# Kernel optimization log

Measured on AMD Instinct MI355X. Metric: run time of the kernel, lower is better.

## Reference

```python
import jax, jax.numpy as jnp
import numpy as np

B, T, DIN, DOUT, RANK, UDIM = 4, 2048, 4096, 4096, 2, 16

def setup_inputs() -> dict:
    key = jax.random.key(0)
    ks = jax.random.split(key, 8)
    return {
        "x": jax.random.normal(ks[0], (B, T, DIN), jnp.float32),
        "W": jax.random.normal(ks[1], (DOUT, DIN), jnp.float32) * 0.02,
        "b": jax.random.normal(ks[2], (DOUT,), jnp.float32) * 0.02,
        "U": jax.random.normal(ks[3], (DOUT, RANK), jnp.float32) * 0.02,
        "S": jax.random.normal(ks[4], (RANK, RANK), jnp.float32),
        "Vh": jax.random.normal(ks[5], (RANK, DIN), jnp.float32) * 0.02,
        "P": jax.random.normal(ks[6], (UDIM, RANK, RANK), jnp.float32),
        "v": jax.random.normal(ks[7], (UDIM,), jnp.float32),
    }

def reference(x, W, b, U, S, Vh, P, v):
    # R = sum_u v[u] * P[u]  (intended meaning of einsum('u,urr->rr'))
    R = jnp.einsum('u,uab->ab', v, P)                 # [rank, rank]
    base = jnp.einsum('btd,od->bto', x, W) + b        # frozen linear
    # x @ delta_W.T with delta_W = U @ S @ R @ Vh, chained low-rank:
    M = U @ S @ R                                     # [out, rank]
    t = jnp.einsum('btd,rd->btr', x, Vh)              # [B, T, rank]
    delta = jnp.einsum('btr,or->bto', t, M)           # [B, T, out]
    return base + delta
```

## Files before the change

### kernel.cpp

```cpp
#include <hip/hip_runtime.h>
#include <hip/hip_bf16.h>
#include <stdint.h>

typedef __hip_bfloat16 bf16;
typedef __attribute__((ext_vector_type(8))) short bf16x8;
typedef __attribute__((ext_vector_type(4))) float f32x4;

static constexpr int Mtot = 8192;
static constexpr int Ktot = 4096;
static constexpr int Ntot = 4096;
static constexpr int BM = 128, BN = 128, BK = 32;

__device__ __forceinline__ void gl_lds16(const void* g, void* l) {
  __builtin_amdgcn_global_load_lds(
      (const __attribute__((address_space(1))) void*)g,
      (__attribute__((address_space(3))) void*)l,
      16, 0, 0);
}

__device__ __forceinline__ uint32_t bf16pair(float a, float b) {
  __hip_bfloat16 ha = __float2bfloat16(a), hb = __float2bfloat16(b);
  uint16_t ia, ib;
  __builtin_memcpy(&ia, &ha, 2);
  __builtin_memcpy(&ib, &hb, 2);
  return (uint32_t)ia | ((uint32_t)ib << 16);
}

__global__ __launch_bounds__(256) void cast_x_kernel(const float* __restrict__ x,
                                                     bf16* __restrict__ xb) {
  size_t gid = (size_t)blockIdx.x * blockDim.x + threadIdx.x;
  size_t d0 = gid * 8;
  const float4 a = ((const float4*)(x + d0))[0];
  const float4 b = ((const float4*)(x + d0))[1];
  uint4 pk;
  pk.x = bf16pair(a.x, a.y);
  pk.y = bf16pair(a.z, a.w);
  pk.z = bf16pair(b.x, b.y);
  pk.w = bf16pair(b.z, b.w);
  ((uint4*)(xb + d0))[0] = pk;
}

__global__ __launch_bounds__(256) void prep_w_kernel(const float* __restrict__ W,
                                                     const float* __restrict__ U,
                                                     const float* __restrict__ S,
                                                     const float* __restrict__ Vh,
                                                     const float* __restrict__ P,
                                                     const float* __restrict__ v,
                                                     bf16* __restrict__ Wp) {
  float R0 = 0.f, R1 = 0.f, R2 = 0.f, R3 = 0.f;
#pragma unroll
  for (int u = 0; u < 16; ++u) {
    float vu = v[u];
    R0 += vu * P[u * 4 + 0];
    R1 += vu * P[u * 4 + 1];
    R2 += vu * P[u * 4 + 2];
    R3 += vu * P[u * 4 + 3];
  }
  float SR00 = S[0] * R0 + S[1] * R2, SR01 = S[0] * R1 + S[1] * R3;
  float SR10 = S[2] * R0 + S[3] * R2, SR11 = S[2] * R1 + S[3] * R3;

  int gid = blockIdx.x * blockDim.x + threadIdx.x;
  int o = gid >> 9;
  int d0 = (gid & 511) << 3;
  float u0 = U[o * 2 + 0], u1 = U[o * 2 + 1];
  float M0 = u0 * SR00 + u1 * SR10;
  float M1 = u0 * SR01 + u1 * SR11;

  const float* wrow = W + (size_t)o * Ktot + d0;
  const float* vh0 = Vh + d0;
  const float* vh1 = Vh + Ktot + d0;
  float val[8];
  const float4 w0 = ((const float4*)wrow)[0];
  const float4 w1 = ((const float4*)wrow)[1];
  const float4 a0 = ((const float4*)vh0)[0];
  const float4 a1 = ((const float4*)vh0)[1];
  const float4 b0 = ((const float4*)vh1)[0];
  const float4 b1 = ((const float4*)vh1)[1];
  val[0] = w0.x + M0 * a0.x + M1 * b0.x;
  val[1] = w0.y + M0 * a0.y + M1 * b0.y;
  val[2] = w0.z + M0 * a0.z + M1 * b0.z;
  val[3] = w0.w + M0 * a0.w + M1 * b0.w;
  val[4] = w1.x + M0 * a1.x + M1 * b1.x;
  val[5] = w1.y + M0 * a1.y + M1 * b1.y;
  val[6] = w1.z + M0 * a1.z + M1 * b1.z;
  val[7] = w1.w + M0 * a1.w + M1 * b1.w;
  uint4 pk;
  pk.x = bf16pair(val[0], val[1]);
  pk.y = bf16pair(val[2], val[3]);
  pk.z = bf16pair(val[4], val[5]);
  pk.w = bf16pair(val[6], val[7]);
  ((uint4*)(Wp + (size_t)o * Ktot + d0))[0] = pk;
}

__global__ __launch_bounds__(256) void gemm_kernel(const bf16* __restrict__ A,
                                                   const bf16* __restrict__ Bt,
                                                   const float* __restrict__ bias,
                                                   float* __restrict__ out) {
  __shared__ __align__(16) bf16 As[BM * BK];
  __shared__ __align__(16) bf16 Bs[BN * BK];

  const int tid = threadIdx.x;
  const int lane = tid & 63;
  const int wv = tid >> 6;
  const int m0 = blockIdx.y * BM;
  const int n0 = blockIdx.x * BN;

  const int lrow = lane >> 2;
  const int lk = (lane & 3) << 3;

  const bf16* ga0 = A + (size_t)(m0 + wv * 32 + lrow) * Ktot + lk;
  const bf16* ga1 = ga0 + (size_t)16 * Ktot;
  const bf16* gb0 = Bt + (size_t)(n0 + wv * 32 + lrow) * Ktot + lk;
  const bf16* gb1 = gb0 + (size_t)16 * Ktot;
  bf16* la0 = &As[(wv * 32) * BK];
  bf16* la1 = &As[(wv * 32 + 16) * BK];
  bf16* lb0 = &Bs[(wv * 32) * BK];
  bf16* lb1 = &Bs[(wv * 32 + 16) * BK];

  const int moff = (wv >> 1) * 64;
  const int noff = (wv & 1) * 64;
  const int fm = lane & 15;
  const int q = lane >> 4;
  const bf16* ra = &As[(moff + fm) * BK + q * 8];
  const bf16* rb = &Bs[(noff + fm) * BK + q * 8];

  f32x4 acc[4][4];
#pragma unroll
  for (int i = 0; i < 4; ++i)
#pragma unroll
    for (int j = 0; j < 4; ++j) acc[i][j] = {0.f, 0.f, 0.f, 0.f};

  for (int kt = 0; kt < Ktot / BK; ++kt) {
    gl_lds16(ga0, la0);
    gl_lds16(ga1, la1);
    gl_lds16(gb0, lb0);
    gl_lds16(gb1, lb1);
    ga0 += BK; ga1 += BK; gb0 += BK; gb1 += BK;
    __syncthreads();

    bf16x8 av[4], bv[4];
#pragma unroll
    for (int i = 0; i < 4; ++i) av[i] = *(const bf16x8*)(ra + i * 16 * BK);
#pragma unroll
    for (int j = 0; j < 4; ++j) bv[j] = *(const bf16x8*)(rb + j * 16 * BK);
#pragma unroll
    for (int i = 0; i < 4; ++i)
#pragma unroll
      for (int j = 0; j < 4; ++j)
        acc[i][j] = __builtin_amdgcn_mfma_f32_16x16x32_bf16(av[i], bv[j], acc[i][j], 0, 0, 0);
    __syncthreads();
  }

#pragma unroll
  for (int j = 0; j < 4; ++j) {
    const int gn = n0 + noff + j * 16 + fm;
    const float bj = bias[gn];
#pragma unroll
    for (int i = 0; i < 4; ++i) {
      const int gm = m0 + moff + i * 16 + q * 4;
#pragma unroll
      for (int r = 0; r < 4; ++r) {
        out[(size_t)(gm + r) * Ntot + gn] = acc[i][j][r] + bj;
      }
    }
  }
}

extern "C" void kernel_launch(void* const* d_in, const int* in_sizes, int n_in,
                              void* d_out, int out_size, void* d_ws, size_t ws_size,
                              hipStream_t stream) {
  const float* x  = (const float*)d_in[0];
  const float* W  = (const float*)d_in[1];
  const float* b  = (const float*)d_in[2];
  const float* U  = (const float*)d_in[3];
  const float* S  = (const float*)d_in[4];
  const float* Vh = (const float*)d_in[5];
  const float* P  = (const float*)d_in[6];
  const float* v  = (const float*)d_in[7];
  float* out = (float*)d_out;

  bf16* xb = (bf16*)d_ws;
  bf16* Wp = (bf16*)((char*)d_ws + (size_t)Mtot * Ktot * 2);

  cast_x_kernel<<<(Mtot * Ktot / 8) / 256, 256, 0, stream>>>(x, xb);
  prep_w_kernel<<<(Ntot * Ktot / 8) / 256, 256, 0, stream>>>(W, U, S, Vh, P, v, Wp);

  dim3 grid(Ntot / BN, Mtot / BM);
  gemm_kernel<<<grid, 256, 0, stream>>>(xb, Wp, b, out);
}
```

Before: 625.7 us.

## Double-buffer GEMM LDS tiles, XOR-swizzle LDS layout, merge prep kernels

```diff
diff --git a/kernel.cpp b/kernel.cpp
--- a/kernel.cpp
+++ b/kernel.cpp
@@ -10,6 +10,9 @@
 static constexpr int Ktot = 4096;
 static constexpr int Ntot = 4096;
 static constexpr int BM = 128, BN = 128, BK = 32;
+static constexpr int NK = Ktot / BK;
+static constexpr int CAST_BLOCKS = (Mtot * Ktot / 8) / 256;
+static constexpr int PREP_BLOCKS = (Ntot * Ktot / 8) / 256;
 
 __device__ __forceinline__ void gl_lds16(const void* g, void* l) {
   __builtin_amdgcn_global_load_lds(
@@ -26,78 +29,78 @@
   return (uint32_t)ia | ((uint32_t)ib << 16);
 }
 
-__global__ __launch_bounds__(256) void cast_x_kernel(const float* __restrict__ x,
-                                                     bf16* __restrict__ xb) {
-  size_t gid = (size_t)blockIdx.x * blockDim.x + threadIdx.x;
-  size_t d0 = gid * 8;
-  const float4 a = ((const float4*)(x + d0))[0];
-  const float4 b = ((const float4*)(x + d0))[1];
-  uint4 pk;
-  pk.x = bf16pair(a.x, a.y);
-  pk.y = bf16pair(a.z, a.w);
-  pk.z = bf16pair(b.x, b.y);
-  pk.w = bf16pair(b.z, b.w);
-  ((uint4*)(xb + d0))[0] = pk;
-}
-
-__global__ __launch_bounds__(256) void prep_w_kernel(const float* __restrict__ W,
-                                                     const float* __restrict__ U,
-                                                     const float* __restrict__ S,
-                                                     const float* __restrict__ Vh,
-                                                     const float* __restrict__ P,
-                                                     const float* __restrict__ v,
-                                                     bf16* __restrict__ Wp) {
-  float R0 = 0.f, R1 = 0.f, R2 = 0.f, R3 = 0.f;
-#pragma unroll
-  for (int u = 0; u < 16; ++u) {
-    float vu = v[u];
-    R0 += vu * P[u * 4 + 0];
-    R1 += vu * P[u * 4 + 1];
-    R2 += vu * P[u * 4 + 2];
-    R3 += vu * P[u * 4 + 3];
+__global__ __launch_bounds__(256) void prep_kernel(const float* __restrict__ x,
+                                                   bf16* __restrict__ xb,
+                                                   const float* __restrict__ W,
+                                                   const float* __restrict__ U,
+                                                   const float* __restrict__ S,
+                                                   const float* __restrict__ Vh,
+                                                   const float* __restrict__ P,
+                                                   const float* __restrict__ v,
+                                                   bf16* __restrict__ Wp) {
+  const int bid = blockIdx.x;
+  if (bid < CAST_BLOCKS) {
+    size_t gid = (size_t)bid * 256 + threadIdx.x;
+    size_t d0 = gid * 8;
+    const float4 a = ((const float4*)(x + d0))[0];
+    const float4 b = ((const float4*)(x + d0))[1];
+    uint4 pk;
+    pk.x = bf16pair(a.x, a.y);
+    pk.y = bf16pair(a.z, a.w);
+    pk.z = bf16pair(b.x, b.y);
+    pk.w = bf16pair(b.z, b.w);
+    ((uint4*)(xb + d0))[0] = pk;
+  } else {
+    float R0 = 0.f, R1 = 0.f, R2 = 0.f, R3 = 0.f;
+#pragma unroll
+    for (int u = 0; u < 16; ++u) {
+      float vu = v[u];
+      R0 += vu * P[u * 4 + 0];
+      R1 += vu * P[u * 4 + 1];
+      R2 += vu * P[u * 4 + 2];
+      R3 += vu * P[u * 4 + 3];
+    }
+    float SR00 = S[0] * R0 + S[1] * R2, SR01 = S[0] * R1 + S[1] * R3;
+    float SR10 = S[2] * R0 + S[3] * R2, SR11 = S[2] * R1 + S[3] * R3;
+
+    int gid = (bid - CAST_BLOCKS) * 256 + threadIdx.x;
+    int o = gid >> 9;
+    int d0 = (gid & 511) << 3;
+    float u0 = U[o * 2 + 0], u1 = U[o * 2 + 1];
+    float M0 = u0 * SR00 + u1 * SR10;
+    float M1 = u0 * SR01 + u1 * SR11;
+
+    const float* wrow = W + (size_t)o * Ktot + d0;
+    const float4 w0 = ((const float4*)wrow)[0];
+    const float4 w1 = ((const float4*)wrow)[1];
+    const float4 a0 = ((const float4*)(Vh + d0))[0];
+    const float4 a1 = ((const float4*)(Vh + d0))[1];
+    const float4 b0 = ((const float4*)(Vh + Ktot + d0))[0];
+    const float4 b1 = ((const float4*)(Vh + Ktot + d0))[1];
+    float val[8];
+    val[0] = w0.x + M0 * a0.x + M1 * b0.x;
+    val[1] = w0.y + M0 * a0.y + M1 * b0.y;
+    val[2] = w0.z + M0 * a0.z + M1 * b0.z;
+    val[3] = w0.w + M0 * a0.w + M1 * b0.w;
+    val[4] = w1.x + M0 * a1.x + M1 * b1.x;
+    val[5] = w1.y + M0 * a1.y + M1 * b1.y;
+    val[6] = w1.z + M0 * a1.z + M1 * b1.z;
+    val[7] = w1.w + M0 * a1.w + M1 * b1.w;
+    uint4 pk;
+    pk.x = bf16pair(val[0], val[1]);
+    pk.y = bf16pair(val[2], val[3]);
+    pk.z = bf16pair(val[4], val[5]);
+    pk.w = bf16pair(val[6], val[7]);
+    ((uint4*)(Wp + (size_t)o * Ktot + d0))[0] = pk;
   }
-  float SR00 = S[0] * R0 + S[1] * R2, SR01 = S[0] * R1 + S[1] * R3;
-  float SR10 = S[2] * R0 + S[3] * R2, SR11 = S[2] * R1 + S[3] * R3;
-
-  int gid = blockIdx.x * blockDim.x + threadIdx.x;
-  int o = gid >> 9;
-  int d0 = (gid & 511) << 3;
-  float u0 = U[o * 2 + 0], u1 = U[o * 2 + 1];
-  float M0 = u0 * SR00 + u1 * SR10;
-  float M1 = u0 * SR01 + u1 * SR11;
-
-  const float* wrow = W + (size_t)o * Ktot + d0;
-  const float* vh0 = Vh + d0;
-  const float* vh1 = Vh + Ktot + d0;
-  float val[8];
-  const float4 w0 = ((const float4*)wrow)[0];
-  const float4 w1 = ((const float4*)wrow)[1];
-  const float4 a0 = ((const float4*)vh0)[0];
-  const float4 a1 = ((const float4*)vh0)[1];
-  const float4 b0 = ((const float4*)vh1)[0];
-  const float4 b1 = ((const float4*)vh1)[1];
-  val[0] = w0.x + M0 * a0.x + M1 * b0.x;
-  val[1] = w0.y + M0 * a0.y + M1 * b0.y;
-  val[2] = w0.z + M0 * a0.z + M1 * b0.z;
-  val[3] = w0.w + M0 * a0.w + M1 * b0.w;
-  val[4] = w1.x + M0 * a1.x + M1 * b1.x;
-  val[5] = w1.y + M0 * a1.y + M1 * b1.y;
-  val[6] = w1.z + M0 * a1.z + M1 * b1.z;
-  val[7] = w1.w + M0 * a1.w + M1 * b1.w;
-  uint4 pk;
-  pk.x = bf16pair(val[0], val[1]);
-  pk.y = bf16pair(val[2], val[3]);
-  pk.z = bf16pair(val[4], val[5]);
-  pk.w = bf16pair(val[6], val[7]);
-  ((uint4*)(Wp + (size_t)o * Ktot + d0))[0] = pk;
 }
 
 __global__ __launch_bounds__(256) void gemm_kernel(const bf16* __restrict__ A,
                                                    const bf16* __restrict__ Bt,
                                                    const float* __restrict__ bias,
                                                    float* __restrict__ out) {
-  __shared__ __align__(16) bf16 As[BM * BK];
-  __shared__ __align__(16) bf16 Bs[BN * BK];
+  __shared__ __align__(16) bf16 As[2][BM * BK];
+  __shared__ __align__(16) bf16 Bs[2][BN * BK];
 
   const int tid = threadIdx.x;
   const int lane = tid & 63;
@@ -106,23 +109,20 @@
   const int n0 = blockIdx.x * BN;
 
   const int lrow = lane >> 2;
-  const int lk = (lane & 3) << 3;
+  const int lk = (((lane & 3) ^ ((lrow >> 1) & 3)) << 3);
 
   const bf16* ga0 = A + (size_t)(m0 + wv * 32 + lrow) * Ktot + lk;
   const bf16* ga1 = ga0 + (size_t)16 * Ktot;
   const bf16* gb0 = Bt + (size_t)(n0 + wv * 32 + lrow) * Ktot + lk;
   const bf16* gb1 = gb0 + (size_t)16 * Ktot;
-  bf16* la0 = &As[(wv * 32) * BK];
-  bf16* la1 = &As[(wv * 32 + 16) * BK];
-  bf16* lb0 = &Bs[(wv * 32) * BK];
-  bf16* lb1 = &Bs[(wv * 32 + 16) * BK];
+  const int laoff0 = (wv * 32) * BK;
+  const int laoff1 = (wv * 32 + 16) * BK;
 
   const int moff = (wv >> 1) * 64;
   const int noff = (wv & 1) * 64;
   const int fm = lane & 15;
   const int q = lane >> 4;
-  const bf16* ra = &As[(moff + fm) * BK + q * 8];
-  const bf16* rb = &Bs[(noff + fm) * BK + q * 8];
+  const int sw = ((q ^ ((fm >> 1) & 3)) << 3);
 
   f32x4 acc[4][4];
 #pragma unroll
@@ -130,24 +130,39 @@
 #pragma unroll
     for (int j = 0; j < 4; ++j) acc[i][j] = {0.f, 0.f, 0.f, 0.f};
 
-  for (int kt = 0; kt < Ktot / BK; ++kt) {
-    gl_lds16(ga0, la0);
-    gl_lds16(ga1, la1);
-    gl_lds16(gb0, lb0);
-    gl_lds16(gb1, lb1);
-    ga0 += BK; ga1 += BK; gb0 += BK; gb1 += BK;
-    __syncthreads();
-
+  gl_lds16(ga0, &As[0][laoff0]);
+  gl_lds16(ga1, &As[0][laoff1]);
+  gl_lds16(gb0, &Bs[0][laoff0]);
+  gl_lds16(gb1, &Bs[0][laoff1]);
+  ga0 += BK; ga1 += BK; gb0 += BK; gb1 += BK;
+  __syncthreads();
+
+  for (int kt = 0; kt < NK; ++kt) {
+    const int cur = kt & 1;
+    if (kt + 1 < NK) {
+      const int nxt = cur ^ 1;
+      gl_lds16(ga0, &As[nxt][laoff0]);
+      gl_lds16(ga1, &As[nxt][laoff1]);
+      gl_lds16(gb0, &Bs[nxt][laoff0]);
+      gl_lds16(gb1, &Bs[nxt][laoff1]);
+      ga0 += BK; ga1 += BK; gb0 += BK; gb1 += BK;
+    }
+
+    const bf16* pa = &As[cur][0];
+    const bf16* pb = &Bs[cur][0];
     bf16x8 av[4], bv[4];
 #pragma unroll
-    for (int i = 0; i < 4; ++i) av[i] = *(const bf16x8*)(ra + i * 16 * BK);
-#pragma unroll
-    for (int j = 0; j < 4; ++j) bv[j] = *(const bf16x8*)(rb + j * 16 * BK);
+    for (int i = 0; i < 4; ++i)
+      av[i] = *(const bf16x8*)(pa + (moff + i * 16 + fm) * BK + sw);
+#pragma unroll
+    for (int j = 0; j < 4; ++j)
+      bv[j] = *(const bf16x8*)(pb + (noff + j * 16 + fm) * BK + sw);
 #pragma unroll
     for (int i = 0; i < 4; ++i)
 #pragma unroll
       for (int j = 0; j < 4; ++j)
         acc[i][j] = __builtin_amdgcn_mfma_f32_16x16x32_bf16(av[i], bv[j], acc[i][j], 0, 0, 0);
+
     __syncthreads();
   }
 
@@ -182,8 +197,7 @@
   bf16* xb = (bf16*)d_ws;
   bf16* Wp = (bf16*)((char*)d_ws + (size_t)Mtot * Ktot * 2);
 
-  cast_x_kernel<<<(Mtot * Ktot / 8) / 256, 256, 0, stream>>>(x, xb);
-  prep_w_kernel<<<(Ntot * Ktot / 8) / 256, 256, 0, stream>>>(W, U, S, Vh, P, v, Wp);
+  prep_kernel<<<CAST_BLOCKS + PREP_BLOCKS, 256, 0, stream>>>(x, xb, W, U, S, Vh, P, v, Wp);
 
   dim3 grid(Ntot / BN, Mtot / BM);
   gemm_kernel<<<grid, 256, 0, stream>>>(xb, Wp, b, out);
```

New measurement: 614.4 us. Within noise of the previous version (-1.8%).
